# Optimization experiments

Hardware: AMD Instinct MI355X
Metric: run time of the kernel (lower is better)

## Reference

```python
import jax, jax.numpy as jnp
import numpy as np

B, N, E, H, R, L, VOCAB, KINDS = 8, 4096, 524288, 128, 8, 2, 100000, 8


def setup_inputs() -> dict:
    key = jax.random.key(0)
    ks = jax.random.split(key, 12)
    concept_ids = jax.random.randint(ks[0], (B, N), 1, VOCAB)  # avoid padding_idx 0
    kind_ids = jax.random.randint(ks[1], (B, N), 0, KINDS)
    node_mask = jnp.ones((B, N), dtype=jnp.int32)
    # edges constrained within each batch block (module assumes per-subgraph edges)
    e_batch = jax.random.randint(ks[2], (E,), 0, B)
    src = e_batch * N + jax.random.randint(ks[3], (E,), 0, N)
    dst = e_batch * N + jax.random.randint(ks[4], (E,), 0, N)
    edge_index = jnp.stack([src, dst], axis=0)
    edge_type = jax.random.randint(ks[5], (E,), 0, R)
    s = 0.02
    concept_emb = jax.random.normal(ks[6], (VOCAB, H), jnp.float32) * s
    concept_emb = concept_emb.at[0].set(0.0)  # padding_idx=0
    kind_emb = jax.random.normal(ks[7], (KINDS, H), jnp.float32) * s
    proj_W = jax.random.normal(ks[8], (H, H), jnp.float32) * s
    proj_b = jnp.zeros((H,), jnp.float32)
    self_W = jax.random.normal(ks[9], (L, H, H), jnp.float32) * s
    self_b = jnp.zeros((L, H), jnp.float32)
    rel_W = jax.random.normal(ks[10], (L, R, H, H), jnp.float32) * s
    return dict(pkg_node_concept_ids=concept_ids, pkg_node_kind_ids=kind_ids,
                pkg_node_mask=node_mask, pkg_edge_index=edge_index,
                pkg_edge_type=edge_type, concept_emb=concept_emb, kind_emb=kind_emb,
                proj_W=proj_W, proj_b=proj_b, self_W=self_W, self_b=self_b, rel_W=rel_W)


def reference(pkg_node_concept_ids, pkg_node_kind_ids, pkg_node_mask,
              pkg_edge_index, pkg_edge_type, concept_emb, kind_emb,
              proj_W, proj_b, self_W, self_b, rel_W):
    b, n = pkg_node_concept_ids.shape
    num_nodes = b * n
    # input embedding + projection (dropout = identity in eval)
    x = concept_emb[pkg_node_concept_ids] + kind_emb[pkg_node_kind_ids]  # [B,N,H]
    x = jnp.einsum('bnh,gh->bng', x, proj_W) + proj_b
    x = x.reshape(num_nodes, -1)  # packed node states [B*N, H]
    src, dst = pkg_edge_index[0], pkg_edge_index[1]
    deg = jax.ops.segment_sum(jnp.ones_like(src, dtype=x.dtype), dst,
                              num_segments=num_nodes)[:, None]
    deg = jnp.maximum(deg, 1.0)
    n_layers, n_rel = rel_W.shape[0], rel_W.shape[1]
    for l in range(n_layers):
        xs = x[src]  # [E,H] gather
        msgs = jnp.zeros_like(xs)
        for r in range(n_rel):
            msgs = msgs + jnp.where((pkg_edge_type == r)[:, None],
                                    xs @ rel_W[l, r].T, 0.0)
        agg = jax.ops.segment_sum(msgs, dst, num_segments=num_nodes) / deg
        x = jax.nn.relu(x @ self_W[l].T + self_b[l] + agg)
    out = x.reshape(b, n, -1) * pkg_node_mask[..., None].astype(x.dtype)
    return out
```

## Files before the change

kernel.cpp:

```cpp
#include <hip/hip_runtime.h>
#include <hip/hip_bf16.h>

#define NODES 32768
#define HD 128
#define NE 524288
#define NR 8
#define NS 262144
#define PASSB 65536

typedef unsigned int u32;
typedef unsigned short u16;
typedef __attribute__((ext_vector_type(8))) short bf16x8;
typedef __attribute__((ext_vector_type(4))) float f32x4;

#define XH_OFF   (0u)
#define XL_OFF   (8u<<20)
#define XH2_OFF  (16u<<20)
#define XL2_OFF  (24u<<20)
#define ADJ_OFF  (32u<<20)
#define RP_OFF   (34u<<20)
#define CUR_OFF  (36u<<20)
#define BSUM_OFF (37u<<20)
#define BP_OFF   (38u<<20)

#define BP_LAYER 294912
#define PP_ELEM  589824

__device__ __forceinline__ float bflo(u32 u){ union{u32 i;float f;}c; c.i=u<<16; return c.f; }
__device__ __forceinline__ float bfhi(u32 u){ union{u32 i;float f;}c; c.i=u&0xffff0000u; return c.f; }
__device__ __forceinline__ u16 f2bf(float f){
  u32 u=__float_as_uint(f);
  u32 r=u + 0x7fffu + ((u>>16)&1u);
  return (u16)(r>>16);
}
__device__ __forceinline__ float bf2f(u16 h){ return __uint_as_float(((u32)h)<<16); }

__device__ __forceinline__ void gl_lds16(const void* g, void* l){
  __builtin_amdgcn_global_load_lds((const __attribute__((address_space(1))) u32*)g,
                                   (__attribute__((address_space(3))) u32*)l, 16, 0, 0);
}

__global__ void prep_w(const float* __restrict__ rW, const float* __restrict__ sW,
                       const float* __restrict__ pWg, u16* __restrict__ Bp)
{
  int idx=blockIdx.x*256+threadIdx.x;
  if(idx<294912){
    int l=idx/147456;
    int rem=idx%147456;
    int t=rem>>14;
    int kn=rem&16383;
    int k=kn>>7, n=kn&127;
    float w;
    if(t<8) w=rW[(((size_t)l*NR+t)*HD+n)*HD+k];
    else    w=sW[((size_t)l*HD+n)*HD+k];
    u16* base=Bp+(size_t)l*BP_LAYER+(size_t)t*32768;
    int ks=k>>5, q=(k>>3)&3, j=k&7;
    size_t off=((size_t)ks*128+n)*32+q*8+j;
    u16 hb=f2bf(w);
    u16 lb=f2bf(w-bf2f(hb));
    base[off]=hb;
    base[off+16384]=lb;
  } else {
    int kn=idx-294912;
    int k=kn>>7, n=kn&127;
    float w=pWg[(size_t)n*HD+k];
    u16* base=Bp+PP_ELEM;
    int ks=k>>5, q=(k>>3)&3, j=k&7;
    size_t off=((size_t)ks*128+n)*32+q*8+j;
    u16 hb=f2bf(w);
    u16 lb=f2bf(w-bf2f(hb));
    base[off]=hb;
    base[off+16384]=lb;
  }
}

__global__ __launch_bounds__(256,2) void embed_mfma(
    const int* __restrict__ cid, const int* __restrict__ kid,
    const float* __restrict__ cemb, const float* __restrict__ kemb,
    const u16* __restrict__ PP, const float* __restrict__ pb,
    u16* __restrict__ xh, u16* __restrict__ xl)
{
  __shared__ u16 Atile[2][128*128];
  const int tid=threadIdx.x;
  const int wave=tid>>6, lane=tid&63;
  const int wm=wave>>1, wn=wave&1;
  const int q=lane>>4;
  const int d0=blockIdx.x*128;

  { int r=tid>>1, half=tid&1;
    int ci=cid[d0+r], ki=kid[d0+r];
    const float* cp=cemb+(size_t)ci*HD+half*64;
    const float* kp=kemb+(size_t)ki*HD+half*64;
#pragma unroll
    for(int cc=0;cc<8;cc++){
      float4 a0=*(const float4*)(cp+cc*8);
      float4 a1=*(const float4*)(cp+cc*8+4);
      float4 b0=*(const float4*)(kp+cc*8);
      float4 b1=*(const float4*)(kp+cc*8+4);
      float v[8]={a0.x+b0.x,a0.y+b0.y,a0.z+b0.z,a0.w+b0.w,
                  a1.x+b1.x,a1.y+b1.y,a1.z+b1.z,a1.w+b1.w};
      u16 hb[8], lb[8];
#pragma unroll
      for(int j=0;j<8;j++){ hb[j]=f2bf(v[j]); lb[j]=f2bf(v[j]-bf2f(hb[j])); }
      int chunk=half*8+cc;
      int dst=r*128+(chunk^(r&15))*8;
      uint4 hv={(u32)hb[0]|((u32)hb[1]<<16),(u32)hb[2]|((u32)hb[3]<<16),
                (u32)hb[4]|((u32)hb[5]<<16),(u32)hb[6]|((u32)hb[7]<<16)};
      uint4 lv={(u32)lb[0]|((u32)lb[1]<<16),(u32)lb[2]|((u32)lb[3]<<16),
                (u32)lb[4]|((u32)lb[5]<<16),(u32)lb[6]|((u32)lb[7]<<16)};
      *(uint4*)&Atile[0][dst]=hv;
      *(uint4*)&Atile[1][dst]=lv;
    }
  }
  __syncthreads();

  f32x4 acc[4][4];
#pragma unroll
  for(int a=0;a<4;a++)
#pragma unroll
    for(int b=0;b<4;b++) acc[a][b]=(f32x4){0.f,0.f,0.f,0.f};

#pragma unroll
  for(int ks=0;ks<4;ks++){
    bf16x8 ah[4];
#pragma unroll
    for(int tm=0;tm<4;tm++){
      int m=wm*64+tm*16+(lane&15);
      ah[tm]=*(const bf16x8*)&Atile[0][m*128+(((ks*4)+q)^(m&15))*8];
    }
#pragma unroll
    for(int s=0;s<2;s++){
      const u16* Bb=PP+s*16384;
#pragma unroll
      for(int tn=0;tn<4;tn++){
        int n=wn*64+tn*16+(lane&15);
        bf16x8 bfr=*(const bf16x8*)&Bb[((size_t)ks*128+n)*32+q*8];
#pragma unroll
        for(int tm=0;tm<4;tm++)
          acc[tm][tn]=__builtin_amdgcn_mfma_f32_16x16x32_bf16(ah[tm],bfr,acc[tm][tn],0,0,0);
      }
    }
  }
#pragma unroll
  for(int ks=0;ks<4;ks++){
    bf16x8 al[4];
#pragma unroll
    for(int tm=0;tm<4;tm++){
      int m=wm*64+tm*16+(lane&15);
      al[tm]=*(const bf16x8*)&Atile[1][m*128+(((ks*4)+q)^(m&15))*8];
    }
#pragma unroll
    for(int tn=0;tn<4;tn++){
      int n=wn*64+tn*16+(lane&15);
      bf16x8 bfr=*(const bf16x8*)&PP[((size_t)ks*128+n)*32+q*8];
#pragma unroll
      for(int tm=0;tm<4;tm++)
        acc[tm][tn]=__builtin_amdgcn_mfma_f32_16x16x32_bf16(al[tm],bfr,acc[tm][tn],0,0,0);
    }
  }

  __syncthreads();
  { u16* Sh=(u16*)Atile[0];
    u16* Sl=(u16*)Atile[1];
#pragma unroll
    for(int tn=0;tn<4;tn++){
      int n=wn*64+tn*16+(lane&15);
      float b=pb[n];
#pragma unroll
      for(int tm=0;tm<4;tm++){
        int rbase=wm*64+tm*16+q*4;
#pragma unroll
        for(int r=0;r<4;r++){
          float v=acc[tm][tn][r]+b;
          u16 hb=f2bf(v);
          u16 lb=f2bf(v-bf2f(hb));
          int row=rbase+r;
          u32 ab=(u32)(row*256+n*2);
          ab^=((u32)((row>>2)&3))<<5;
          Sh[ab>>1]=hb;
          Sl[ab>>1]=lb;
        }
      }
    }
  }
  __syncthreads();
  { const char* S0=(const char*)Atile[0];
    const char* S1=(const char*)Atile[1];
    char* xhb=(char*)(xh+(size_t)d0*HD);
    char* xlb=(char*)(xl+(size_t)d0*HD);
#pragma unroll
    for(int i=0;i<8;i++){
      u32 byte=(u32)(i*256+tid)*16;
      u32 row=byte>>8;
      u32 lb2=byte^((((row>>2)&3))<<5);
      *(uint4*)(xhb+byte)=*(const uint4*)(S0+lb2);
      *(uint4*)(xlb+byte)=*(const uint4*)(S1+lb2);
    }
  }
}

__global__ void count_deg2(const int* __restrict__ dst, const int* __restrict__ et,
                           u32* __restrict__ cnt){
  int e=blockIdx.x*256+threadIdx.x;
  int t=et[e];
  int key=(t>>1)*PASSB + dst[e]*2 + (t&1);
  atomicAdd(&cnt[key],1u);
}

__global__ void scan1(u32* __restrict__ cnt, u32* __restrict__ rp, u32* __restrict__ bsum){
  __shared__ u32 sh[256];
  int t=threadIdx.x; int base=blockIdx.x*256;
  u32 v=cnt[base+t]; sh[t]=v;
  cnt[base+t]=0u;
  __syncthreads();
  for(int off=1;off<256;off<<=1){
    u32 tv=(t>=off)?sh[t-off]:0u; __syncthreads();
    sh[t]+=tv; __syncthreads();
  }
  rp[base+t]=sh[t]-v;
  if(t==255) bsum[blockIdx.x]=sh[255];
}

__global__ void scan2b(u32* __restrict__ bsum, u32* __restrict__ rp){
  __shared__ u32 sh[256];
  int t=threadIdx.x;
  u32 v0=bsum[t*4+0],v1=bsum[t*4+1],v2=bsum[t*4+2],v3=bsum[t*4+3];
  u32 s=v0+v1+v2+v3;
  sh[t]=s; __syncthreads();
  for(int off=1;off<256;off<<=1){
    u32 tv=(t>=off)?sh[t-off]:0u; __syncthreads();
    sh[t]+=tv; __syncthreads();
  }
  u32 ex=sh[t]-s;
  bsum[t*4+0]=ex; bsum[t*4+1]=ex+v0; bsum[t*4+2]=ex+v0+v1; bsum[t*4+3]=ex+v0+v1+v2;
  if(t==0) rp[NS]=NE;
  if(t==255) bsum[1024]=0u;
}

__global__ void scatter_edges2(const int* __restrict__ src, const int* __restrict__ dst,
                               const int* __restrict__ et, const u32* __restrict__ rp,
                               const u32* __restrict__ bsum,
                               u32* __restrict__ cur, u32* __restrict__ adj){
  int e=blockIdx.x*256+threadIdx.x;
  int t=et[e];
  int d=dst[e];
  int key=(t>>1)*PASSB + d*2 + (t&1);
  u32 pos=atomicAdd(&cur[key],1u);
  u32 val=(u32)src[e] | (((u32)(((t&1)<<5)|(d&31)))<<15);
  adj[rp[key]+bsum[key>>8]+pos]=val;
}

#define FLUSH2(rw) do{ \
  u32 u0=__float_as_uint(v0), u1=__float_as_uint(v1); \
  u32 t0=u0&0xffff0000u, t1=u1&0xffff0000u; \
  u32 hp=t1|(u0>>16); \
  float l0f=v0-__uint_as_float(t0), l1f=v1-__uint_as_float(t1); \
  u32 w0b=__float_as_uint(l0f), w1b=__float_as_uint(l1f); \
  u32 lp=(w1b&0xffff0000u)|(w0b>>16); \
  int fw=(rw)*64 + (((lane>>2)^((rw)&15))<<2) + (lane&3); \
  ((u32*)As[0])[fw]=hp; \
  ((u32*)As[1])[fw]=lp; \
}while(0)

__global__ __launch_bounds__(256,4) void fused_layer(
    const u16* __restrict__ xh, const u16* __restrict__ xl,
    const u16* __restrict__ Bp,
    const u32* __restrict__ rp, const u32* __restrict__ bsum,
    const u32* __restrict__ adj,
    const float* __restrict__ sb, const int* __restrict__ mask,
    u16* __restrict__ oh, u16* __restrict__ ol, float* __restrict__ outf, int last)
{
  __shared__ u16 As[2][64*128];
  __shared__ float sdeg[32];
  const int tid=threadIdx.x;
  const int wave=tid>>6, lane=tid&63;
  const int q=lane>>4;
  const int d0=blockIdx.x*32;
  const u32* xh32=(const u32*)xh;

  f32x4 accR[2][2], accS[2][2];
#pragma unroll
  for(int a=0;a<2;a++)
#pragma unroll
    for(int b=0;b<2;b++){ accR[a][b]=(f32x4){0.f,0.f,0.f,0.f}; accS[a][b]=(f32x4){0.f,0.f,0.f,0.f}; }

  for(int p=0;p<4;p++){
    { uint4 zz={0u,0u,0u,0u};
#pragma unroll
      for(int rl=0;rl<2;rl++)
#pragma unroll
        for(int i=0;i<2;i++){
          int row=rl*32+wave*8+i*4+(lane>>4);
          int col16=lane&15;
          *(uint4*)&As[0][row*128+col16*8]=zz;
          *(uint4*)&As[1][row*128+col16*8]=zz;
        }
    }
    { u32 k0=(u32)(p*PASSB + (d0+wave*8)*2);
      u32 begW=rp[k0]+bsum[k0>>8];
      u32 k1=k0+16;
      u32 endW=rp[k1]+bsum[(k1)>>8];
      int currow=-1; float v0=0.f,v1=0.f;
      for(u32 base=begW; base<endW; base+=64){
        int nk=(int)(endW-base); if(nk>64) nk=64;
        u32 adjv=(lane<nk)?adj[base+lane]:0u;
        int i=0;
        for(; i+8<=nk; i+=8){
          u32 ww[8]; u32 hv[8];
#pragma unroll
          for(int j=0;j<8;j++){
            ww[j]=(u32)__builtin_amdgcn_readlane((int)adjv,i+j);
            hv[j]=xh32[(size_t)(ww[j]&0x7fffu)*64+lane];
          }
#pragma unroll
          for(int j=0;j<8;j++){
            int r=(int)(ww[j]>>15);
            if(r!=currow){ if(currow>=0) FLUSH2(currow); currow=r; v0=0.f; v1=0.f; }
            v0+=__uint_as_float(hv[j]<<16);
            v1+=__uint_as_float(hv[j]&0xffff0000u);
          }
        }
        for(; i<nk; i++){
          u32 w=(u32)__builtin_amdgcn_readlane((int)adjv,i);
          u32 h=xh32[(size_t)(w&0x7fffu)*64+lane];
          int r=(int)(w>>15);
          if(r!=currow){ if(currow>=0) FLUSH2(currow); currow=r; v0=0.f; v1=0.f; }
          v0+=__uint_as_float(h<<16);
          v1+=__uint_as_float(h&0xffff0000u);
        }
      }
      if(currow>=0) FLUSH2(currow);
    }
    __syncthreads();
#pragma unroll
    for(int rl=0;rl<2;rl++){
      const u16* Bt=Bp+(size_t)(p*2+rl)*32768;
#pragma unroll
      for(int ks=0;ks<4;ks++){
        bf16x8 ah[2],al[2];
#pragma unroll
        for(int mf=0;mf<2;mf++){
          int ar=rl*32+mf*16+(lane&15);
          int off=ar*128+((((ks<<2)+q)^(ar&15))<<3);
          ah[mf]=*(const bf16x8*)&As[0][off];
          al[mf]=*(const bf16x8*)&As[1][off];
        }
#pragma unroll
        for(int tn=0;tn<2;tn++){
          int n=wave*32+tn*16+(lane&15);
          size_t boff=((size_t)(ks*128+n))*32+q*8;
          bf16x8 bh=*(const bf16x8*)&Bt[boff];
          bf16x8 bl=*(const bf16x8*)&Bt[boff+16384];
#pragma unroll
          for(int mf=0;mf<2;mf++){
            accR[mf][tn]=__builtin_amdgcn_mfma_f32_16x16x32_bf16(ah[mf],bh,accR[mf][tn],0,0,0);
            accR[mf][tn]=__builtin_amdgcn_mfma_f32_16x16x32_bf16(al[mf],bh,accR[mf][tn],0,0,0);
            accR[mf][tn]=__builtin_amdgcn_mfma_f32_16x16x32_bf16(ah[mf],bl,accR[mf][tn],0,0,0);
          }
        }
      }
    }
    __syncthreads();
  }

#pragma unroll
  for(int i=0;i<2;i++){
    int rbase=wave*8+i*4;
    int r=rbase+(lane>>4);
    int g=(lane&15)^(r&15);
    gl_lds16(xh+(size_t)(d0+r)*HD+g*8, &As[0][rbase*128]);
  }
#pragma unroll
  for(int i=0;i<2;i++){
    int rbase=wave*8+i*4;
    int r=rbase+(lane>>4);
    int g=(lane&15)^(r&15);
    gl_lds16(xl+(size_t)(d0+r)*HD+g*8, &As[1][rbase*128]);
  }
  if(tid<32){
    int g=d0+tid; u32 dg=0;
#pragma unroll
    for(int ph=0;ph<4;ph++){
      u32 k=(u32)(ph*PASSB+g*2);
      dg+=(rp[k+2]+bsum[(k+2)>>8])-(rp[k]+bsum[k>>8]);
    }
    sdeg[tid]=1.f/fmaxf((float)dg,1.f);
  }
  __syncthreads();
  { const u16* Bt=Bp+(size_t)8*32768;
#pragma unroll
    for(int ks=0;ks<4;ks++){
      bf16x8 ah[2],al[2];
#pragma unroll
      for(int mf=0;mf<2;mf++){
        int ar=mf*16+(lane&15);
        int off=ar*128+((((ks<<2)+q)^(ar&15))<<3);
        ah[mf]=*(const bf16x8*)&As[0][off];
        al[mf]=*(const bf16x8*)&As[1][off];
      }
#pragma unroll
      for(int tn=0;tn<2;tn++){
        int n=wave*32+tn*16+(lane&15);
        size_t boff=((size_t)(ks*128+n))*32+q*8;
        bf16x8 bh=*(const bf16x8*)&Bt[boff];
        bf16x8 bl=*(const bf16x8*)&Bt[boff+16384];
#pragma unroll
        for(int mf=0;mf<2;mf++){
          accS[mf][tn]=__builtin_amdgcn_mfma_f32_16x16x32_bf16(ah[mf],bh,accS[mf][tn],0,0,0);
          accS[mf][tn]=__builtin_amdgcn_mfma_f32_16x16x32_bf16(al[mf],bh,accS[mf][tn],0,0,0);
          accS[mf][tn]=__builtin_amdgcn_mfma_f32_16x16x32_bf16(ah[mf],bl,accS[mf][tn],0,0,0);
        }
      }
    }
  }

#pragma unroll
  for(int tn=0;tn<2;tn++){
    int n=wave*32+tn*16+(lane&15);
    float bb=sb[n];
    if(last){
#pragma unroll
      for(int mf=0;mf<2;mf++)
#pragma unroll
        for(int rr=0;rr<4;rr++){
          int row=mf*16+q*4+rr;
          float v=fmaxf(accS[mf][tn][rr]+bb+accR[mf][tn][rr]*sdeg[row],0.f);
          v*=(float)mask[d0+row];
          outf[(size_t)(d0+row)*HD+n]=v;
        }
    } else {
#pragma unroll
      for(int mf=0;mf<2;mf++)
#pragma unroll
        for(int rr=0;rr<4;rr++){
          int row=mf*16+q*4+rr;
          float v=fmaxf(accS[mf][tn][rr]+bb+accR[mf][tn][rr]*sdeg[row],0.f);
          u16 hb=f2bf(v);
          u16 lb=f2bf(v-bf2f(hb));
          oh[(size_t)(d0+row)*HD+n]=hb;
          ol[(size_t)(d0+row)*HD+n]=lb;
        }
    }
  }
}

extern "C" void kernel_launch(void* const* d_in, const int* in_sizes, int n_in,
                              void* d_out, int out_size, void* d_ws, size_t ws_size,
                              hipStream_t stream)
{
  (void)in_sizes; (void)n_in; (void)out_size; (void)ws_size;
  const int*   cid =(const int*)  d_in[0];
  const int*   kid =(const int*)  d_in[1];
  const int*   mask=(const int*)  d_in[2];
  const int*   ei  =(const int*)  d_in[3];
  const int*   et  =(const int*)  d_in[4];
  const float* cemb=(const float*)d_in[5];
  const float* kemb=(const float*)d_in[6];
  const float* pW  =(const float*)d_in[7];
  const float* pb  =(const float*)d_in[8];
  const float* sW  =(const float*)d_in[9];
  const float* sb  =(const float*)d_in[10];
  const float* rW  =(const float*)d_in[11];
  float* out=(float*)d_out;
  char*  ws =(char*)d_ws;

  u16* xh =(u16*)(ws+XH_OFF);
  u16* xl =(u16*)(ws+XL_OFF);
  u16* xh2=(u16*)(ws+XH2_OFF);
  u16* xl2=(u16*)(ws+XL2_OFF);
  u32* adj =(u32*)(ws+ADJ_OFF);
  u32* rp  =(u32*)(ws+RP_OFF);
  u32* cur =(u32*)(ws+CUR_OFF);
  u32* bsum=(u32*)(ws+BSUM_OFF);
  u16* Bp  =(u16*)(ws+BP_OFF);
  const int* srcA=ei;
  const int* dstA=ei+NE;

  hipMemsetAsync(cur,0,NS*sizeof(u32),stream);
  prep_w<<<1216,256,0,stream>>>(rW,sW,pW,Bp);
  embed_mfma<<<NODES/128,256,0,stream>>>(cid,kid,cemb,kemb,Bp+PP_ELEM,pb,xh,xl);
  count_deg2<<<NE/256,256,0,stream>>>(dstA,et,cur);
  scan1<<<NS/256,256,0,stream>>>(cur,rp,bsum);
  scan2b<<<1,256,0,stream>>>(bsum,rp);
  scatter_edges2<<<NE/256,256,0,stream>>>(srcA,dstA,et,rp,bsum,cur,adj);

  fused_layer<<<NODES/32,256,0,stream>>>(xh,xl,Bp,rp,bsum,adj,sb,mask,xh2,xl2,out,0);
  fused_layer<<<NODES/32,256,0,stream>>>(xh2,xl2,Bp+BP_LAYER,rp,bsum,adj,sb+HD,mask,xh,xl,out,1);
}
```

Baseline: 301.2 us.

## Use 64-node blocks with LDS float atomics for balanced edge aggregation

The fused layer kernel now handles 64 destination nodes per 512-thread block, using 8 waves in a 2x4 MFMA tile layout. Each wave used to own 8 rows and run a sequential segment-flush accumulation. Now the block's edge range for each pass is split evenly across waves, and messages are accumulated with float atomicAdd into a 128x128 fp32 LDS buffer, which is then converted to hi/lo bf16 tiles. Gathers are double-buffered in groups of 16 to keep more loads in flight. The aim is to remove per-wave load imbalance and expose more memory parallelism. The cost is LDS atomic contention, a larger 64KB LDS footprint that may cut occupancy, and an extra conversion pass. The adjacency row encoding widens to 6 bits to match.

```diff
diff --git a/kernel.cpp b/kernel.cpp
--- a/kernel.cpp
+++ b/kernel.cpp
@@ -246,23 +246,11 @@
   int d=dst[e];
   int key=(t>>1)*PASSB + d*2 + (t&1);
   u32 pos=atomicAdd(&cur[key],1u);
-  u32 val=(u32)src[e] | (((u32)(((t&1)<<5)|(d&31)))<<15);
+  u32 val=(u32)src[e] | (((u32)(((t&1)<<6)|(d&63)))<<15);
   adj[rp[key]+bsum[key>>8]+pos]=val;
 }
 
-#define FLUSH2(rw) do{ \
-  u32 u0=__float_as_uint(v0), u1=__float_as_uint(v1); \
-  u32 t0=u0&0xffff0000u, t1=u1&0xffff0000u; \
-  u32 hp=t1|(u0>>16); \
-  float l0f=v0-__uint_as_float(t0), l1f=v1-__uint_as_float(t1); \
-  u32 w0b=__float_as_uint(l0f), w1b=__float_as_uint(l1f); \
-  u32 lp=(w1b&0xffff0000u)|(w0b>>16); \
-  int fw=(rw)*64 + (((lane>>2)^((rw)&15))<<2) + (lane&3); \
-  ((u32*)As[0])[fw]=hp; \
-  ((u32*)As[1])[fw]=lp; \
-}while(0)
-
-__global__ __launch_bounds__(256,4) void fused_layer(
+__global__ __launch_bounds__(512,4) void fused_layer(
     const u16* __restrict__ xh, const u16* __restrict__ xl,
     const u16* __restrict__ Bp,
     const u32* __restrict__ rp, const u32* __restrict__ bsum,
@@ -270,66 +258,97 @@
     const float* __restrict__ sb, const int* __restrict__ mask,
     u16* __restrict__ oh, u16* __restrict__ ol, float* __restrict__ outf, int last)
 {
-  __shared__ u16 As[2][64*128];
-  __shared__ float sdeg[32];
+  __shared__ float A32[128*128];
+  __shared__ float sdeg[64];
+  u16* As16=(u16*)A32;
+  u32* As32w=(u32*)A32;
   const int tid=threadIdx.x;
   const int wave=tid>>6, lane=tid&63;
+  const int wm=wave>>2, wn=wave&3;
   const int q=lane>>4;
-  const int d0=blockIdx.x*32;
+  const int d0=blockIdx.x*64;
   const u32* xh32=(const u32*)xh;
 
-  f32x4 accR[2][2], accS[2][2];
+  f32x4 accR[2][2];
 #pragma unroll
   for(int a=0;a<2;a++)
 #pragma unroll
-    for(int b=0;b<2;b++){ accR[a][b]=(f32x4){0.f,0.f,0.f,0.f}; accS[a][b]=(f32x4){0.f,0.f,0.f,0.f}; }
+    for(int b=0;b<2;b++) accR[a][b]=(f32x4){0.f,0.f,0.f,0.f};
+
+#define PROC(W,H) do{ \
+    u32 row_=(W)>>15; \
+    float* rb_=&A32[row_*128+lane]; \
+    atomicAdd(rb_,    bflo(H)); \
+    atomicAdd(rb_+64, bfhi(H)); \
+  }while(0)
 
   for(int p=0;p<4;p++){
     { uint4 zz={0u,0u,0u,0u};
 #pragma unroll
-      for(int rl=0;rl<2;rl++)
-#pragma unroll
-        for(int i=0;i<2;i++){
-          int row=rl*32+wave*8+i*4+(lane>>4);
-          int col16=lane&15;
-          *(uint4*)&As[0][row*128+col16*8]=zz;
-          *(uint4*)&As[1][row*128+col16*8]=zz;
-        }
-    }
-    { u32 k0=(u32)(p*PASSB + (d0+wave*8)*2);
-      u32 begW=rp[k0]+bsum[k0>>8];
-      u32 k1=k0+16;
-      u32 endW=rp[k1]+bsum[(k1)>>8];
-      int currow=-1; float v0=0.f,v1=0.f;
-      for(u32 base=begW; base<endW; base+=64){
-        int nk=(int)(endW-base); if(nk>64) nk=64;
+      for(int k2=0;k2<8;k2++) *(uint4*)&A32[k2*2048+tid*4]=zz;
+    }
+    __syncthreads();
+    { u32 kb=(u32)(p*PASSB + d0*2);
+      u32 ke=kb+128u;
+      u32 beg=rp[kb]+bsum[kb>>8];
+      u32 end=rp[ke]+bsum[ke>>8];
+      u32 len=end-beg;
+      u32 wbeg=beg + (len*(u32)wave)/8u;
+      u32 wend=beg + (len*(u32)(wave+1))/8u;
+      for(u32 base=wbeg; base<wend; base+=64u){
+        int nk=(int)(wend-base); if(nk>64) nk=64;
         u32 adjv=(lane<nk)?adj[base+lane]:0u;
-        int i=0;
-        for(; i+8<=nk; i+=8){
-          u32 ww[8]; u32 hv[8];
-#pragma unroll
-          for(int j=0;j<8;j++){
-            ww[j]=(u32)__builtin_amdgcn_readlane((int)adjv,i+j);
-            hv[j]=xh32[(size_t)(ww[j]&0x7fffu)*64+lane];
+        u32 hA[16], hB[16];
+#pragma unroll
+        for(int j=0;j<16;j++) if(j<nk){
+          u32 w=(u32)__builtin_amdgcn_readlane((int)adjv,j);
+          hA[j]=xh32[(size_t)(w&0x7fffu)*64+lane];
+        }
+        for(int i0=0;i0<nk;i0+=32){
+#pragma unroll
+          for(int j=0;j<16;j++) if(i0+16+j<nk){
+            u32 w=(u32)__builtin_amdgcn_readlane((int)adjv,i0+16+j);
+            hB[j]=xh32[(size_t)(w&0x7fffu)*64+lane];
           }
 #pragma unroll
-          for(int j=0;j<8;j++){
-            int r=(int)(ww[j]>>15);
-            if(r!=currow){ if(currow>=0) FLUSH2(currow); currow=r; v0=0.f; v1=0.f; }
-            v0+=__uint_as_float(hv[j]<<16);
-            v1+=__uint_as_float(hv[j]&0xffff0000u);
+          for(int j=0;j<16;j++) if(i0+j<nk){
+            u32 w=(u32)__builtin_amdgcn_readlane((int)adjv,i0+j);
+            PROC(w,hA[j]);
           }
-        }
-        for(; i<nk; i++){
-          u32 w=(u32)__builtin_amdgcn_readlane((int)adjv,i);
-          u32 h=xh32[(size_t)(w&0x7fffu)*64+lane];
-          int r=(int)(w>>15);
-          if(r!=currow){ if(currow>=0) FLUSH2(currow); currow=r; v0=0.f; v1=0.f; }
-          v0+=__uint_as_float(h<<16);
-          v1+=__uint_as_float(h&0xffff0000u);
-        }
-      }
-      if(currow>=0) FLUSH2(currow);
+#pragma unroll
+          for(int j=0;j<16;j++) if(i0+32+j<nk){
+            u32 w=(u32)__builtin_amdgcn_readlane((int)adjv,i0+32+j);
+            hA[j]=xh32[(size_t)(w&0x7fffu)*64+lane];
+          }
+#pragma unroll
+          for(int j=0;j<16;j++) if(i0+16+j<nk){
+            u32 w=(u32)__builtin_amdgcn_readlane((int)adjv,i0+16+j);
+            PROC(w,hB[j]);
+          }
+        }
+      }
+    }
+    __syncthreads();
+    { float c0[16], c1[16];
+#pragma unroll
+      for(int r=0;r<16;r++){
+        int row=wave*16+r;
+        c0[r]=A32[row*128+lane];
+        c1[r]=A32[row*128+64+lane];
+      }
+      __syncthreads();
+#pragma unroll
+      for(int r=0;r<16;r++){
+        int row=wave*16+r;
+        u32 u0=__float_as_uint(c0[r]), u1=__float_as_uint(c1[r]);
+        u32 hp=(u1&0xffff0000u)|(u0>>16);
+        float l0=c0[r]-__uint_as_float(u0&0xffff0000u);
+        float l1=c1[r]-__uint_as_float(u1&0xffff0000u);
+        u32 lp=(__float_as_uint(l1)&0xffff0000u)|(__float_as_uint(l0)>>16);
+        int fw=row*64 + (((lane>>2)^(row&15))<<2) + (lane&3);
+        As32w[fw]=hp;
+        As32w[8192+fw]=lp;
+      }
     }
     __syncthreads();
 #pragma unroll
@@ -340,14 +359,14 @@
         bf16x8 ah[2],al[2];
 #pragma unroll
         for(int mf=0;mf<2;mf++){
-          int ar=rl*32+mf*16+(lane&15);
+          int ar=rl*64+wm*32+mf*16+(lane&15);
           int off=ar*128+((((ks<<2)+q)^(ar&15))<<3);
-          ah[mf]=*(const bf16x8*)&As[0][off];
-          al[mf]=*(const bf16x8*)&As[1][off];
+          ah[mf]=*(const bf16x8*)&As16[off];
+          al[mf]=*(const bf16x8*)&As16[16384+off];
         }
 #pragma unroll
         for(int tn=0;tn<2;tn++){
-          int n=wave*32+tn*16+(lane&15);
+          int n=wn*32+tn*16+(lane&15);
           size_t boff=((size_t)(ks*128+n))*32+q*8;
           bf16x8 bh=*(const bf16x8*)&Bt[boff];
           bf16x8 bl=*(const bf16x8*)&Bt[boff+16384];
@@ -368,16 +387,10 @@
     int rbase=wave*8+i*4;
     int r=rbase+(lane>>4);
     int g=(lane&15)^(r&15);
-    gl_lds16(xh+(size_t)(d0+r)*HD+g*8, &As[0][rbase*128]);
-  }
-#pragma unroll
-  for(int i=0;i<2;i++){
-    int rbase=wave*8+i*4;
-    int r=rbase+(lane>>4);
-    int g=(lane&15)^(r&15);
-    gl_lds16(xl+(size_t)(d0+r)*HD+g*8, &As[1][rbase*128]);
-  }
-  if(tid<32){
+    gl_lds16(xh+(size_t)(d0+r)*HD+g*8, (char*)A32 + rbase*256);
+    gl_lds16(xl+(size_t)(d0+r)*HD+g*8, (char*)A32 + 32768 + rbase*256);
+  }
+  if(tid<64){
     int g=d0+tid; u32 dg=0;
 #pragma unroll
     for(int ph=0;ph<4;ph++){
@@ -387,20 +400,26 @@
     sdeg[tid]=1.f/fmaxf((float)dg,1.f);
   }
   __syncthreads();
+
+  f32x4 accS[2][2];
+#pragma unroll
+  for(int a=0;a<2;a++)
+#pragma unroll
+    for(int b=0;b<2;b++) accS[a][b]=(f32x4){0.f,0.f,0.f,0.f};
   { const u16* Bt=Bp+(size_t)8*32768;
 #pragma unroll
     for(int ks=0;ks<4;ks++){
       bf16x8 ah[2],al[2];
 #pragma unroll
       for(int mf=0;mf<2;mf++){
-        int ar=mf*16+(lane&15);
+        int ar=wm*32+mf*16+(lane&15);
         int off=ar*128+((((ks<<2)+q)^(ar&15))<<3);
-        ah[mf]=*(const bf16x8*)&As[0][off];
-        al[mf]=*(const bf16x8*)&As[1][off];
+        ah[mf]=*(const bf16x8*)&As16[off];
+        al[mf]=*(const bf16x8*)&As16[16384+off];
       }
 #pragma unroll
       for(int tn=0;tn<2;tn++){
-        int n=wave*32+tn*16+(lane&15);
+        int n=wn*32+tn*16+(lane&15);
         size_t boff=((size_t)(ks*128+n))*32+q*8;
         bf16x8 bh=*(const bf16x8*)&Bt[boff];
         bf16x8 bl=*(const bf16x8*)&Bt[boff+16384];
@@ -416,14 +435,14 @@
 
 #pragma unroll
   for(int tn=0;tn<2;tn++){
-    int n=wave*32+tn*16+(lane&15);
+    int n=wn*32+tn*16+(lane&15);
     float bb=sb[n];
     if(last){
 #pragma unroll
       for(int mf=0;mf<2;mf++)
 #pragma unroll
         for(int rr=0;rr<4;rr++){
-          int row=mf*16+q*4+rr;
+          int row=wm*32+mf*16+q*4+rr;
           float v=fmaxf(accS[mf][tn][rr]+bb+accR[mf][tn][rr]*sdeg[row],0.f);
           v*=(float)mask[d0+row];
           outf[(size_t)(d0+row)*HD+n]=v;
@@ -433,7 +452,7 @@
       for(int mf=0;mf<2;mf++)
 #pragma unroll
         for(int rr=0;rr<4;rr++){
-          int row=mf*16+q*4+rr;
+          int row=wm*32+mf*16+q*4+rr;
           float v=fmaxf(accS[mf][tn][rr]+bb+accR[mf][tn][rr]*sdeg[row],0.f);
           u16 hb=f2bf(v);
           u16 lb=f2bf(v-bf2f(hb));
@@ -442,6 +461,7 @@
         }
     }
   }
+#undef PROC
 }
 
 extern "C" void kernel_launch(void* const* d_in, const int* in_sizes, int n_in,
@@ -484,6 +504,6 @@
   scan2b<<<1,256,0,stream>>>(bsum,rp);
   scatter_edges2<<<NE/256,256,0,stream>>>(srcA,dstA,et,rp,bsum,cur,adj);
 
-  fused_layer<<<NODES/32,256,0,stream>>>(xh,xl,Bp,rp,bsum,adj,sb,mask,xh2,xl2,out,0);
-  fused_layer<<<NODES/32,256,0,stream>>>(xh2,xl2,Bp+BP_LAYER,rp,bsum,adj,sb+HD,mask,xh,xl,out,1);
-}
+  fused_layer<<<NODES/64,512,0,stream>>>(xh,xl,Bp,rp,bsum,adj,sb,mask,xh2,xl2,out,0);
+  fused_layer<<<NODES/64,512,0,stream>>>(xh2,xl2,Bp+BP_LAYER,rp,bsum,adj,sb+HD,mask,xh,xl,out,1);
+}
```

After: 1.013 ms. +236.4%, slower.

## Aggregate all relation rows in one pass with single-bf16 messages

Applied to the files above, without the earlier changes.

Edges are regrouped by destination block first and then by relation type, so each block gathers all 8 relation segments for its 32 nodes in a single pass into one 256-row LDS tile instead of four passes of 64 rows. The hi/lo bf16 split of the aggregated messages is dropped, so the relation GEMM uses one MFMA per fragment instead of three. The gather loop is restructured to issue 64 loads up front before accumulating. This cuts MFMA work and per-pass synchronisation, but it enlarges LDS use, lowers launch bounds to 2 blocks per SM, and reduces precision of the aggregated message.

```diff
diff --git a/kernel.cpp b/kernel.cpp
--- a/kernel.cpp
+++ b/kernel.cpp
@@ -203,7 +203,8 @@
                            u32* __restrict__ cnt){
   int e=blockIdx.x*256+threadIdx.x;
   int t=et[e];
-  int key=(t>>1)*PASSB + dst[e]*2 + (t&1);
+  int d=dst[e];
+  int key=(d>>5)*256 + t*32 + (d&31);
   atomicAdd(&cnt[key],1u);
 }
 
@@ -244,25 +245,13 @@
   int e=blockIdx.x*256+threadIdx.x;
   int t=et[e];
   int d=dst[e];
-  int key=(t>>1)*PASSB + d*2 + (t&1);
+  int key=(d>>5)*256 + t*32 + (d&31);
   u32 pos=atomicAdd(&cur[key],1u);
-  u32 val=(u32)src[e] | (((u32)(((t&1)<<5)|(d&31)))<<15);
-  adj[rp[key]+bsum[key>>8]+pos]=val;
-}
-
-#define FLUSH2(rw) do{ \
-  u32 u0=__float_as_uint(v0), u1=__float_as_uint(v1); \
-  u32 t0=u0&0xffff0000u, t1=u1&0xffff0000u; \
-  u32 hp=t1|(u0>>16); \
-  float l0f=v0-__uint_as_float(t0), l1f=v1-__uint_as_float(t1); \
-  u32 w0b=__float_as_uint(l0f), w1b=__float_as_uint(l1f); \
-  u32 lp=(w1b&0xffff0000u)|(w0b>>16); \
-  int fw=(rw)*64 + (((lane>>2)^((rw)&15))<<2) + (lane&3); \
-  ((u32*)As[0])[fw]=hp; \
-  ((u32*)As[1])[fw]=lp; \
-}while(0)
-
-__global__ __launch_bounds__(256,4) void fused_layer(
+  u32 row=(u32)((t<<5)|(d&31));
+  adj[rp[key]+bsum[key>>8]+pos]=(u32)src[e] | (row<<15);
+}
+
+__global__ __launch_bounds__(256,2) void fused_layer(
     const u16* __restrict__ xh, const u16* __restrict__ xl,
     const u16* __restrict__ Bp,
     const u32* __restrict__ rp, const u32* __restrict__ bsum,
@@ -270,7 +259,7 @@
     const float* __restrict__ sb, const int* __restrict__ mask,
     u16* __restrict__ oh, u16* __restrict__ ol, float* __restrict__ outf, int last)
 {
-  __shared__ u16 As[2][64*128];
+  __shared__ u16 As16[256*128];
   __shared__ float sdeg[32];
   const int tid=threadIdx.x;
   const int wave=tid>>6, lane=tid&63;
@@ -278,115 +267,109 @@
   const int d0=blockIdx.x*32;
   const u32* xh32=(const u32*)xh;
 
-  f32x4 accR[2][2], accS[2][2];
+  { uint4 zz={0u,0u,0u,0u};
+    uint4* p4=(uint4*)As16;
+#pragma unroll
+    for(int i=0;i<16;i++) p4[wave*1024 + i*64 + lane]=zz;
+  }
+
+#define FLUSH1(rw) do{ \
+    u32 u0=__float_as_uint(v0), u1=__float_as_uint(v1); \
+    u32 hp=(u1&0xffff0000u)|(u0>>16); \
+    int fw=(rw)*64 + (((lane>>2)^((rw)&15))<<2) + (lane&3); \
+    ((u32*)As16)[fw]=hp; \
+  }while(0)
+  { u32 kb=(u32)(blockIdx.x*256 + wave*64);
+    u32 beg=rp[kb]+bsum[kb>>8];
+    u32 ke=kb+64u;
+    u32 end=rp[ke]+bsum[ke>>8];
+    int currow=-1; float v0=0.f,v1=0.f;
+    for(u32 base=beg; base<end; base+=64u){
+      int nk=(int)(end-base); if(nk>64) nk=64;
+      u32 adjv=(lane<nk)?adj[base+lane]:0u;
+      u32 hA[32], hB[32];
+#pragma unroll
+      for(int j=0;j<32;j++)
+        hA[j]=xh32[(size_t)((u32)__builtin_amdgcn_readlane((int)adjv,j)&0x7fffu)*64+lane];
+#pragma unroll
+      for(int j=0;j<32;j++)
+        hB[j]=xh32[(size_t)((u32)__builtin_amdgcn_readlane((int)adjv,j+32)&0x7fffu)*64+lane];
+#pragma unroll
+      for(int j=0;j<32;j++){
+        if(j<nk){
+          u32 w=(u32)__builtin_amdgcn_readlane((int)adjv,j);
+          int r=(int)(w>>15);
+          if(r!=currow){ if(currow>=0) FLUSH1(currow); currow=r; v0=0.f; v1=0.f; }
+          v0+=bflo(hA[j]); v1+=bfhi(hA[j]);
+        }
+      }
+#pragma unroll
+      for(int j=0;j<32;j++){
+        if(j+32<nk){
+          u32 w=(u32)__builtin_amdgcn_readlane((int)adjv,j+32);
+          int r=(int)(w>>15);
+          if(r!=currow){ if(currow>=0) FLUSH1(currow); currow=r; v0=0.f; v1=0.f; }
+          v0+=bflo(hB[j]); v1+=bfhi(hB[j]);
+        }
+      }
+    }
+    if(currow>=0) FLUSH1(currow);
+  }
+#undef FLUSH1
+  __syncthreads();
+
+  f32x4 accR[2][2];
 #pragma unroll
   for(int a=0;a<2;a++)
 #pragma unroll
-    for(int b=0;b<2;b++){ accR[a][b]=(f32x4){0.f,0.f,0.f,0.f}; accS[a][b]=(f32x4){0.f,0.f,0.f,0.f}; }
-
-  for(int p=0;p<4;p++){
-    { uint4 zz={0u,0u,0u,0u};
-#pragma unroll
-      for(int rl=0;rl<2;rl++)
-#pragma unroll
-        for(int i=0;i<2;i++){
-          int row=rl*32+wave*8+i*4+(lane>>4);
-          int col16=lane&15;
-          *(uint4*)&As[0][row*128+col16*8]=zz;
-          *(uint4*)&As[1][row*128+col16*8]=zz;
-        }
-    }
-    { u32 k0=(u32)(p*PASSB + (d0+wave*8)*2);
-      u32 begW=rp[k0]+bsum[k0>>8];
-      u32 k1=k0+16;
-      u32 endW=rp[k1]+bsum[(k1)>>8];
-      int currow=-1; float v0=0.f,v1=0.f;
-      for(u32 base=begW; base<endW; base+=64){
-        int nk=(int)(endW-base); if(nk>64) nk=64;
-        u32 adjv=(lane<nk)?adj[base+lane]:0u;
-        int i=0;
-        for(; i+8<=nk; i+=8){
-          u32 ww[8]; u32 hv[8];
-#pragma unroll
-          for(int j=0;j<8;j++){
-            ww[j]=(u32)__builtin_amdgcn_readlane((int)adjv,i+j);
-            hv[j]=xh32[(size_t)(ww[j]&0x7fffu)*64+lane];
-          }
-#pragma unroll
-          for(int j=0;j<8;j++){
-            int r=(int)(ww[j]>>15);
-            if(r!=currow){ if(currow>=0) FLUSH2(currow); currow=r; v0=0.f; v1=0.f; }
-            v0+=__uint_as_float(hv[j]<<16);
-            v1+=__uint_as_float(hv[j]&0xffff0000u);
-          }
-        }
-        for(; i<nk; i++){
-          u32 w=(u32)__builtin_amdgcn_readlane((int)adjv,i);
-          u32 h=xh32[(size_t)(w&0x7fffu)*64+lane];
-          int r=(int)(w>>15);
-          if(r!=currow){ if(currow>=0) FLUSH2(currow); currow=r; v0=0.f; v1=0.f; }
-          v0+=__uint_as_float(h<<16);
-          v1+=__uint_as_float(h&0xffff0000u);
-        }
-      }
-      if(currow>=0) FLUSH2(currow);
-    }
-    __syncthreads();
-#pragma unroll
-    for(int rl=0;rl<2;rl++){
-      const u16* Bt=Bp+(size_t)(p*2+rl)*32768;
-#pragma unroll
-      for(int ks=0;ks<4;ks++){
-        bf16x8 ah[2],al[2];
-#pragma unroll
-        for(int mf=0;mf<2;mf++){
-          int ar=rl*32+mf*16+(lane&15);
-          int off=ar*128+((((ks<<2)+q)^(ar&15))<<3);
-          ah[mf]=*(const bf16x8*)&As[0][off];
-          al[mf]=*(const bf16x8*)&As[1][off];
-        }
-#pragma unroll
-        for(int tn=0;tn<2;tn++){
-          int n=wave*32+tn*16+(lane&15);
-          size_t boff=((size_t)(ks*128+n))*32+q*8;
-          bf16x8 bh=*(const bf16x8*)&Bt[boff];
-          bf16x8 bl=*(const bf16x8*)&Bt[boff+16384];
-#pragma unroll
-          for(int mf=0;mf<2;mf++){
-            accR[mf][tn]=__builtin_amdgcn_mfma_f32_16x16x32_bf16(ah[mf],bh,accR[mf][tn],0,0,0);
-            accR[mf][tn]=__builtin_amdgcn_mfma_f32_16x16x32_bf16(al[mf],bh,accR[mf][tn],0,0,0);
-            accR[mf][tn]=__builtin_amdgcn_mfma_f32_16x16x32_bf16(ah[mf],bl,accR[mf][tn],0,0,0);
-          }
-        }
-      }
-    }
-    __syncthreads();
-  }
+    for(int b=0;b<2;b++) accR[a][b]=(f32x4){0.f,0.f,0.f,0.f};
+#pragma unroll
+  for(int rl=0;rl<8;rl++){
+    const u16* Bt=Bp+(size_t)rl*32768;
+#pragma unroll
+    for(int ks=0;ks<4;ks++){
+      bf16x8 ah[2];
+#pragma unroll
+      for(int mf=0;mf<2;mf++){
+        int ar=rl*32+mf*16+(lane&15);
+        ah[mf]=*(const bf16x8*)&As16[ar*128+((((ks<<2)+q)^(ar&15))<<3)];
+      }
+#pragma unroll
+      for(int tn=0;tn<2;tn++){
+        int n=wave*32+tn*16+(lane&15);
+        bf16x8 bh=*(const bf16x8*)&Bt[((size_t)(ks*128+n))*32+q*8];
+#pragma unroll
+        for(int mf=0;mf<2;mf++)
+          accR[mf][tn]=__builtin_amdgcn_mfma_f32_16x16x32_bf16(ah[mf],bh,accR[mf][tn],0,0,0);
+      }
+    }
+  }
+  __syncthreads();
 
 #pragma unroll
   for(int i=0;i<2;i++){
     int rbase=wave*8+i*4;
     int r=rbase+(lane>>4);
     int g=(lane&15)^(r&15);
-    gl_lds16(xh+(size_t)(d0+r)*HD+g*8, &As[0][rbase*128]);
-  }
-#pragma unroll
-  for(int i=0;i<2;i++){
-    int rbase=wave*8+i*4;
-    int r=rbase+(lane>>4);
-    int g=(lane&15)^(r&15);
-    gl_lds16(xl+(size_t)(d0+r)*HD+g*8, &As[1][rbase*128]);
+    gl_lds16(xh+(size_t)(d0+r)*HD+g*8, &As16[rbase*128]);
+    gl_lds16(xl+(size_t)(d0+r)*HD+g*8, &As16[(32+rbase)*128]);
   }
   if(tid<32){
     int g=d0+tid; u32 dg=0;
 #pragma unroll
-    for(int ph=0;ph<4;ph++){
-      u32 k=(u32)(ph*PASSB+g*2);
-      dg+=(rp[k+2]+bsum[(k+2)>>8])-(rp[k]+bsum[k>>8]);
+    for(int et=0;et<8;et++){
+      u32 k=(u32)(blockIdx.x*256 + et*32 + tid);
+      dg+=(rp[k+1]+bsum[(k+1)>>8])-(rp[k]+bsum[k>>8]);
     }
     sdeg[tid]=1.f/fmaxf((float)dg,1.f);
   }
   __syncthreads();
+
+  f32x4 accS[2][2];
+#pragma unroll
+  for(int a=0;a<2;a++)
+#pragma unroll
+    for(int b=0;b<2;b++) accS[a][b]=(f32x4){0.f,0.f,0.f,0.f};
   { const u16* Bt=Bp+(size_t)8*32768;
 #pragma unroll
     for(int ks=0;ks<4;ks++){
@@ -394,9 +377,9 @@
 #pragma unroll
       for(int mf=0;mf<2;mf++){
         int ar=mf*16+(lane&15);
-        int off=ar*128+((((ks<<2)+q)^(ar&15))<<3);
-        ah[mf]=*(const bf16x8*)&As[0][off];
-        al[mf]=*(const bf16x8*)&As[1][off];
+        int sw=((((ks<<2)+q)^(ar&15))<<3);
+        ah[mf]=*(const bf16x8*)&As16[ar*128+sw];
+        al[mf]=*(const bf16x8*)&As16[(32+ar)*128+sw];
       }
 #pragma unroll
       for(int tn=0;tn<2;tn++){
```

Result: slower. 307.4 us (+2.1%).

## Double waves per block in fused GNN layer and halve embed tile

Applied to the files above, without the earlier changes.

The fused layer kernel now runs 512 threads (8 waves) per 32-node block instead of 256. Each wave gathers edges for 4 destination rows instead of 8 and owns one 16-row by 32-column MFMA tile instead of a 2x2 set. The xh and xl tile loads are split between the two halves of the block. The embed kernel processes 64 nodes per block with half the LDS, allowing higher occupancy. The aim is more parallelism for latency-bound edge gathers, at the cost of more waves contending for LDS and possible occupancy limits at 512 threads.

```diff
diff --git a/kernel.cpp b/kernel.cpp
--- a/kernel.cpp
+++ b/kernel.cpp
@@ -74,25 +74,25 @@
   }
 }
 
-__global__ __launch_bounds__(256,2) void embed_mfma(
+__global__ __launch_bounds__(256,4) void embed_mfma(
     const int* __restrict__ cid, const int* __restrict__ kid,
     const float* __restrict__ cemb, const float* __restrict__ kemb,
     const u16* __restrict__ PP, const float* __restrict__ pb,
     u16* __restrict__ xh, u16* __restrict__ xl)
 {
-  __shared__ u16 Atile[2][128*128];
+  __shared__ u16 Atile[2][64*128];
   const int tid=threadIdx.x;
   const int wave=tid>>6, lane=tid&63;
   const int wm=wave>>1, wn=wave&1;
   const int q=lane>>4;
-  const int d0=blockIdx.x*128;
-
-  { int r=tid>>1, half=tid&1;
+  const int d0=blockIdx.x*64;
+
+  { int r=tid>>2, q4=tid&3;
     int ci=cid[d0+r], ki=kid[d0+r];
-    const float* cp=cemb+(size_t)ci*HD+half*64;
-    const float* kp=kemb+(size_t)ki*HD+half*64;
-#pragma unroll
-    for(int cc=0;cc<8;cc++){
+    const float* cp=cemb+(size_t)ci*HD+q4*32;
+    const float* kp=kemb+(size_t)ki*HD+q4*32;
+#pragma unroll
+    for(int cc=0;cc<4;cc++){
       float4 a0=*(const float4*)(cp+cc*8);
       float4 a1=*(const float4*)(cp+cc*8+4);
       float4 b0=*(const float4*)(kp+cc*8);
@@ -102,7 +102,7 @@
       u16 hb[8], lb[8];
 #pragma unroll
       for(int j=0;j<8;j++){ hb[j]=f2bf(v[j]); lb[j]=f2bf(v[j]-bf2f(hb[j])); }
-      int chunk=half*8+cc;
+      int chunk=q4*4+cc;
       int dst=r*128+(chunk^(r&15))*8;
       uint4 hv={(u32)hb[0]|((u32)hb[1]<<16),(u32)hb[2]|((u32)hb[3]<<16),
                 (u32)hb[4]|((u32)hb[5]<<16),(u32)hb[6]|((u32)hb[7]<<16)};
@@ -114,18 +114,18 @@
   }
   __syncthreads();
 
-  f32x4 acc[4][4];
-#pragma unroll
-  for(int a=0;a<4;a++)
+  f32x4 acc[2][4];
+#pragma unroll
+  for(int a=0;a<2;a++)
 #pragma unroll
     for(int b=0;b<4;b++) acc[a][b]=(f32x4){0.f,0.f,0.f,0.f};
 
 #pragma unroll
   for(int ks=0;ks<4;ks++){
-    bf16x8 ah[4];
-#pragma unroll
-    for(int tm=0;tm<4;tm++){
-      int m=wm*64+tm*16+(lane&15);
+    bf16x8 ah[2];
+#pragma unroll
+    for(int tm=0;tm<2;tm++){
+      int m=wm*32+tm*16+(lane&15);
       ah[tm]=*(const bf16x8*)&Atile[0][m*128+(((ks*4)+q)^(m&15))*8];
     }
 #pragma unroll
@@ -136,17 +136,17 @@
         int n=wn*64+tn*16+(lane&15);
         bf16x8 bfr=*(const bf16x8*)&Bb[((size_t)ks*128+n)*32+q*8];
 #pragma unroll
-        for(int tm=0;tm<4;tm++)
+        for(int tm=0;tm<2;tm++)
           acc[tm][tn]=__builtin_amdgcn_mfma_f32_16x16x32_bf16(ah[tm],bfr,acc[tm][tn],0,0,0);
       }
     }
   }
 #pragma unroll
   for(int ks=0;ks<4;ks++){
-    bf16x8 al[4];
-#pragma unroll
-    for(int tm=0;tm<4;tm++){
-      int m=wm*64+tm*16+(lane&15);
+    bf16x8 al[2];
+#pragma unroll
+    for(int tm=0;tm<2;tm++){
+      int m=wm*32+tm*16+(lane&15);
       al[tm]=*(const bf16x8*)&Atile[1][m*128+(((ks*4)+q)^(m&15))*8];
     }
 #pragma unroll
@@ -154,7 +154,7 @@
       int n=wn*64+tn*16+(lane&15);
       bf16x8 bfr=*(const bf16x8*)&PP[((size_t)ks*128+n)*32+q*8];
 #pragma unroll
-      for(int tm=0;tm<4;tm++)
+      for(int tm=0;tm<2;tm++)
         acc[tm][tn]=__builtin_amdgcn_mfma_f32_16x16x32_bf16(al[tm],bfr,acc[tm][tn],0,0,0);
     }
   }
@@ -167,8 +167,8 @@
       int n=wn*64+tn*16+(lane&15);
       float b=pb[n];
 #pragma unroll
-      for(int tm=0;tm<4;tm++){
-        int rbase=wm*64+tm*16+q*4;
+      for(int tm=0;tm<2;tm++){
+        int rbase=wm*32+tm*16+q*4;
 #pragma unroll
         for(int r=0;r<4;r++){
           float v=acc[tm][tn][r]+b;
@@ -189,7 +189,7 @@
     char* xhb=(char*)(xh+(size_t)d0*HD);
     char* xlb=(char*)(xl+(size_t)d0*HD);
 #pragma unroll
-    for(int i=0;i<8;i++){
+    for(int i=0;i<4;i++){
       u32 byte=(u32)(i*256+tid)*16;
       u32 row=byte>>8;
       u32 lb2=byte^((((row>>2)&3))<<5);
@@ -262,7 +262,7 @@
   ((u32*)As[1])[fw]=lp; \
 }while(0)
 
-__global__ __launch_bounds__(256,4) void fused_layer(
+__global__ __launch_bounds__(512,4) void fused_layer(
     const u16* __restrict__ xh, const u16* __restrict__ xl,
     const u16* __restrict__ Bp,
     const u32* __restrict__ rp, const u32* __restrict__ bsum,
@@ -274,32 +274,29 @@
   __shared__ float sdeg[32];
   const int tid=threadIdx.x;
   const int wave=tid>>6, lane=tid&63;
+  const int wm=wave>>2, wn=wave&3;
   const int q=lane>>4;
   const int d0=blockIdx.x*32;
   const u32* xh32=(const u32*)xh;
 
-  f32x4 accR[2][2], accS[2][2];
-#pragma unroll
-  for(int a=0;a<2;a++)
-#pragma unroll
-    for(int b=0;b<2;b++){ accR[a][b]=(f32x4){0.f,0.f,0.f,0.f}; accS[a][b]=(f32x4){0.f,0.f,0.f,0.f}; }
+  f32x4 accR[2];
+  accR[0]=(f32x4){0.f,0.f,0.f,0.f};
+  accR[1]=(f32x4){0.f,0.f,0.f,0.f};
 
   for(int p=0;p<4;p++){
     { uint4 zz={0u,0u,0u,0u};
 #pragma unroll
-      for(int rl=0;rl<2;rl++)
-#pragma unroll
-        for(int i=0;i<2;i++){
-          int row=rl*32+wave*8+i*4+(lane>>4);
-          int col16=lane&15;
-          *(uint4*)&As[0][row*128+col16*8]=zz;
-          *(uint4*)&As[1][row*128+col16*8]=zz;
-        }
-    }
-    { u32 k0=(u32)(p*PASSB + (d0+wave*8)*2);
+      for(int rl=0;rl<2;rl++){
+        int row=rl*32+wave*4+(lane>>4);
+        int col16=lane&15;
+        *(uint4*)&As[0][row*128+col16*8]=zz;
+        *(uint4*)&As[1][row*128+col16*8]=zz;
+      }
+    }
+    { u32 k0=(u32)(p*PASSB + (d0+wave*4)*2);
       u32 begW=rp[k0]+bsum[k0>>8];
-      u32 k1=k0+16;
-      u32 endW=rp[k1]+bsum[(k1)>>8];
+      u32 k1=k0+8;
+      u32 endW=rp[k1]+bsum[k1>>8];
       int currow=-1; float v0=0.f,v1=0.f;
       for(u32 base=begW; base<endW; base+=64){
         int nk=(int)(endW-base); if(nk>64) nk=64;
@@ -337,26 +334,19 @@
       const u16* Bt=Bp+(size_t)(p*2+rl)*32768;
 #pragma unroll
       for(int ks=0;ks<4;ks++){
-        bf16x8 ah[2],al[2];
-#pragma unroll
-        for(int mf=0;mf<2;mf++){
-          int ar=rl*32+mf*16+(lane&15);
-          int off=ar*128+((((ks<<2)+q)^(ar&15))<<3);
-          ah[mf]=*(const bf16x8*)&As[0][off];
-          al[mf]=*(const bf16x8*)&As[1][off];
-        }
+        int ar=rl*32+wm*16+(lane&15);
+        int off=ar*128+((((ks<<2)+q)^(ar&15))<<3);
+        bf16x8 ah=*(const bf16x8*)&As[0][off];
+        bf16x8 al=*(const bf16x8*)&As[1][off];
 #pragma unroll
         for(int tn=0;tn<2;tn++){
-          int n=wave*32+tn*16+(lane&15);
+          int n=wn*32+tn*16+(lane&15);
           size_t boff=((size_t)(ks*128+n))*32+q*8;
           bf16x8 bh=*(const bf16x8*)&Bt[boff];
           bf16x8 bl=*(const bf16x8*)&Bt[boff+16384];
-#pragma unroll
-          for(int mf=0;mf<2;mf++){
-            accR[mf][tn]=__builtin_amdgcn_mfma_f32_16x16x32_bf16(ah[mf],bh,accR[mf][tn],0,0,0);
-            accR[mf][tn]=__builtin_amdgcn_mfma_f32_16x16x32_bf16(al[mf],bh,accR[mf][tn],0,0,0);
-            accR[mf][tn]=__builtin_amdgcn_mfma_f32_16x16x32_bf16(ah[mf],bl,accR[mf][tn],0,0,0);
-          }
+          accR[tn]=__builtin_amdgcn_mfma_f32_16x16x32_bf16(ah,bh,accR[tn],0,0,0);
+          accR[tn]=__builtin_amdgcn_mfma_f32_16x16x32_bf16(al,bh,accR[tn],0,0,0);
+          accR[tn]=__builtin_amdgcn_mfma_f32_16x16x32_bf16(ah,bl,accR[tn],0,0,0);
         }
       }
     }
@@ -365,17 +355,11 @@
 
 #pragma unroll
   for(int i=0;i<2;i++){
-    int rbase=wave*8+i*4;
+    int rbase=(wave&3)*8+i*4;
     int r=rbase+(lane>>4);
     int g=(lane&15)^(r&15);
-    gl_lds16(xh+(size_t)(d0+r)*HD+g*8, &As[0][rbase*128]);
-  }
-#pragma unroll
-  for(int i=0;i<2;i++){
-    int rbase=wave*8+i*4;
-    int r=rbase+(lane>>4);
-    int g=(lane&15)^(r&15);
-    gl_lds16(xl+(size_t)(d0+r)*HD+g*8, &As[1][rbase*128]);
+    if(wave<4) gl_lds16(xh+(size_t)(d0+r)*HD+g*8, &As[0][rbase*128]);
+    else       gl_lds16(xl+(size_t)(d0+r)*HD+g*8, &As[1][rbase*128]);
   }
   if(tid<32){
     int g=d0+tid; u32 dg=0;
@@ -387,59 +371,52 @@
     sdeg[tid]=1.f/fmaxf((float)dg,1.f);
   }
   __syncthreads();
+
+  f32x4 accS[2];
+  accS[0]=(f32x4){0.f,0.f,0.f,0.f};
+  accS[1]=(f32x4){0.f,0.f,0.f,0.f};
   { const u16* Bt=Bp+(size_t)8*32768;
 #pragma unroll
     for(int ks=0;ks<4;ks++){
-      bf16x8 ah[2],al[2];
-#pragma unroll
-      for(int mf=0;mf<2;mf++){
-        int ar=mf*16+(lane&15);
-        int off=ar*128+((((ks<<2)+q)^(ar&15))<<3);
-        ah[mf]=*(const bf16x8*)&As[0][off];
-        al[mf]=*(const bf16x8*)&As[1][off];
-      }
+      int ar=wm*16+(lane&15);
+      int off=ar*128+((((ks<<2)+q)^(ar&15))<<3);
+      bf16x8 ah=*(const bf16x8*)&As[0][off];
+      bf16x8 al=*(const bf16x8*)&As[1][off];
 #pragma unroll
       for(int tn=0;tn<2;tn++){
-        int n=wave*32+tn*16+(lane&15);
+        int n=wn*32+tn*16+(lane&15);
         size_t boff=((size_t)(ks*128+n))*32+q*8;
         bf16x8 bh=*(const bf16x8*)&Bt[boff];
         bf16x8 bl=*(const bf16x8*)&Bt[boff+16384];
-#pragma unroll
-        for(int mf=0;mf<2;mf++){
-          accS[mf][tn]=__builtin_amdgcn_mfma_f32_16x16x32_bf16(ah[mf],bh,accS[mf][tn],0,0,0);
-          accS[mf][tn]=__builtin_amdgcn_mfma_f32_16x16x32_bf16(al[mf],bh,accS[mf][tn],0,0,0);
-          accS[mf][tn]=__builtin_amdgcn_mfma_f32_16x16x32_bf16(ah[mf],bl,accS[mf][tn],0,0,0);
-        }
+        accS[tn]=__builtin_amdgcn_mfma_f32_16x16x32_bf16(ah,bh,accS[tn],0,0,0);
+        accS[tn]=__builtin_amdgcn_mfma_f32_16x16x32_bf16(al,bh,accS[tn],0,0,0);
+        accS[tn]=__builtin_amdgcn_mfma_f32_16x16x32_bf16(ah,bl,accS[tn],0,0,0);
       }
     }
   }
 
 #pragma unroll
   for(int tn=0;tn<2;tn++){
-    int n=wave*32+tn*16+(lane&15);
+    int n=wn*32+tn*16+(lane&15);
     float bb=sb[n];
     if(last){
 #pragma unroll
-      for(int mf=0;mf<2;mf++)
-#pragma unroll
-        for(int rr=0;rr<4;rr++){
-          int row=mf*16+q*4+rr;
-          float v=fmaxf(accS[mf][tn][rr]+bb+accR[mf][tn][rr]*sdeg[row],0.f);
-          v*=(float)mask[d0+row];
-          outf[(size_t)(d0+row)*HD+n]=v;
-        }
+      for(int rr=0;rr<4;rr++){
+        int row=wm*16+q*4+rr;
+        float v=fmaxf(accS[tn][rr]+bb+accR[tn][rr]*sdeg[row],0.f);
+        v*=(float)mask[d0+row];
+        outf[(size_t)(d0+row)*HD+n]=v;
+      }
     } else {
 #pragma unroll
-      for(int mf=0;mf<2;mf++)
-#pragma unroll
-        for(int rr=0;rr<4;rr++){
-          int row=mf*16+q*4+rr;
-          float v=fmaxf(accS[mf][tn][rr]+bb+accR[mf][tn][rr]*sdeg[row],0.f);
-          u16 hb=f2bf(v);
-          u16 lb=f2bf(v-bf2f(hb));
-          oh[(size_t)(d0+row)*HD+n]=hb;
-          ol[(size_t)(d0+row)*HD+n]=lb;
-        }
+      for(int rr=0;rr<4;rr++){
+        int row=wm*16+q*4+rr;
+        float v=fmaxf(accS[tn][rr]+bb+accR[tn][rr]*sdeg[row],0.f);
+        u16 hb=f2bf(v);
+        u16 lb=f2bf(v-bf2f(hb));
+        oh[(size_t)(d0+row)*HD+n]=hb;
+        ol[(size_t)(d0+row)*HD+n]=lb;
+      }
     }
   }
 }
@@ -478,12 +455,12 @@
 
   hipMemsetAsync(cur,0,NS*sizeof(u32),stream);
   prep_w<<<1216,256,0,stream>>>(rW,sW,pW,Bp);
-  embed_mfma<<<NODES/128,256,0,stream>>>(cid,kid,cemb,kemb,Bp+PP_ELEM,pb,xh,xl);
+  embed_mfma<<<NODES/64,256,0,stream>>>(cid,kid,cemb,kemb,Bp+PP_ELEM,pb,xh,xl);
   count_deg2<<<NE/256,256,0,stream>>>(dstA,et,cur);
   scan1<<<NS/256,256,0,stream>>>(cur,rp,bsum);
   scan2b<<<1,256,0,stream>>>(bsum,rp);
   scatter_edges2<<<NE/256,256,0,stream>>>(srcA,dstA,et,rp,bsum,cur,adj);
 
-  fused_layer<<<NODES/32,256,0,stream>>>(xh,xl,Bp,rp,bsum,adj,sb,mask,xh2,xl2,out,0);
-  fused_layer<<<NODES/32,256,0,stream>>>(xh2,xl2,Bp+BP_LAYER,rp,bsum,adj,sb+HD,mask,xh,xl,out,1);
-}
+  fused_layer<<<NODES/32,512,0,stream>>>(xh,xl,Bp,rp,bsum,adj,sb,mask,(u16*)xh2,(u16*)xl2,out,0);
+  fused_layer<<<NODES/32,512,0,stream>>>(xh2,xl2,Bp+BP_LAYER,rp,bsum,adj,sb+HD,mask,(u16*)xh,(u16*)xl,out,1);
+}
```

After: 373.3 us. +24.0%, slower.
